# Optimization experiments

Measured on AMD Instinct MI355X. Metric: run time of the kernel, lower is better.

Reference implementation:

```python
import jax, jax.numpy as jnp
import numpy as np

CONF_THRES = 0.4
IOU_THRES = 0.45
MAX_DET = 1000
MAX_WH = 7680.0  # class offset for non-agnostic NMS (yolov5 convention)
K = 2048         # pre-NMS candidate cap (>= MAX_DET)


def setup_inputs() -> dict:
    key = jax.random.key(0)
    k1, k2, k3, k4 = jax.random.split(key, 4)
    # uint8-valued image, stored as int32 (values 0..255)
    img = jax.random.randint(k1, (640, 640, 3), 0, 256, dtype=jnp.int32)
    B, N, NC = 8, 25200, 80
    xy = jax.random.uniform(k2, (B, N, 2)) * 640.0          # box centers in pixels
    wh = jax.random.uniform(k3, (B, N, 2)) * 80.0 + 4.0     # box sizes
    sc = jax.random.uniform(k4, (B, N, 1 + NC))             # objectness + class scores
    pred = jnp.concatenate([xy, wh, sc], axis=-1)           # [B, N, 85]
    return {"img": img, "pred": pred}


def _xywh2xyxy(x):
    xy, wh = x[..., :2], x[..., 2:4]
    return jnp.concatenate([xy - wh * 0.5, xy + wh * 0.5], axis=-1)


def _box_iou(a, b):
    # a: [K,4], b: [K,4] in xyxy
    lt = jnp.maximum(a[:, None, :2], b[None, :, :2])
    rb = jnp.minimum(a[:, None, 2:], b[None, :, 2:])
    wh = jnp.clip(rb - lt, 0.0)
    inter = wh[..., 0] * wh[..., 1]
    area_a = (a[:, 2] - a[:, 0]) * (a[:, 3] - a[:, 1])
    area_b = (b[:, 2] - b[:, 0]) * (b[:, 3] - b[:, 1])
    return inter / (area_a[:, None] + area_b[None, :] - inter + 1e-7)


def _nms_single(p):
    # p: [N, 5+nc]
    boxes = _xywh2xyxy(p[:, :4])                 # [N,4]
    conf_all = p[:, 5:] * p[:, 4:5]              # obj * cls
    conf = jnp.max(conf_all, axis=-1)            # best-class confidence [N]
    cls = jnp.argmax(conf_all, axis=-1).astype(p.dtype)
    scores = jnp.where(conf > CONF_THRES, conf, -1.0)
    # top-K candidates (score-sorted, padding gets score -1)
    top_s, idx = jax.lax.top_k(scores, K)
    b = boxes[idx]                               # [K,4] raw boxes
    c = cls[idx]                                 # [K] class ids (float)
    b_off = b + (c * MAX_WH)[:, None]            # class-offset boxes (agnostic_nms=False)
    iou = _box_iou(b_off, b_off)                 # [K,K]
    keep = top_s > CONF_THRES
    ar = jnp.arange(K)

    def body(i, keep):
        sup = keep[i] & (iou[i] > IOU_THRES) & (ar > i)
        return keep & jnp.logical_not(sup)

    keep = jax.lax.fori_loop(0, K, body, keep)
    fs = jnp.where(keep, top_s, -1.0)
    sel_s, sel = jax.lax.top_k(fs, MAX_DET)
    det = jnp.concatenate([b[sel], sel_s[:, None], c[sel][:, None]], axis=-1)  # [MAX_DET,6]
    return jnp.where((sel_s > CONF_THRES)[:, None], det, 0.0)


def reference(img, pred):
    # process_image: HWC -> CHW, BGR->RGB flip, float, /255, add batch dim
    x = img.astype(jnp.float32).transpose(2, 0, 1)[::-1] / 255.0
    x = x[None]                                  # [1,3,640,640]
    det = jax.vmap(_nms_single)(pred)[0]         # non_max_suppression(pred, ...)[0]
    return det, x
```

## Files before the change

### kernel.cpp

```cpp
#include <hip/hip_runtime.h>
#include <stdint.h>

#define N_ANCH 25200
#define NCLS   80
#define KSEL   2048
#define MAXDET 1000
#define CONF_T 0.4f
#define IOU_T  0.45f
#define MAX_WH 7680.0f
#define HBINS  512
#define HBASE  0xBE00u
#define NCAND_MAX 4096
#define NSB    788
#define NIB    400
#define SUPCAP 224

#define WS_SELSCORE  0
#define WS_SELBOX    8192
#define WS_DETCAND   40960
#define WS_CNT       92160
#define WS_KEYS      92480
#define WS_CLS       193280
#define WS_MASK      294912
#define WS_MTT       819200
#define WS_F         1343488
#define WS_DONE      1343744
#define WS_CAND      294912

#define ST_U32(p, v) __hip_atomic_store((p), (v), __ATOMIC_RELAXED, __HIP_MEMORY_SCOPE_AGENT)

__global__ void __launch_bounds__(256)
prep_kernel(const float* __restrict__ pred0, uint32_t* __restrict__ keys,
            int* __restrict__ cls, uint32_t* __restrict__ cnt,
            uint32_t* __restrict__ fglob, uint32_t* __restrict__ done) {
    int tid = threadIdx.x;
    if (blockIdx.x == 0) {
        if (tid < 64) fglob[tid] = 0u;
        if (tid == 64) *cnt = 0u;
        if (tid == 65) *done = 0u;
    }
    int lane = tid & 63, wave = tid >> 6;
    int g = lane >> 3, l = lane & 7;
    int a = blockIdx.x * 32 + wave * 8 + g;
    if (a >= N_ANCH) return;
    const float* p = pred0 + (size_t)a * 85;
    float obj = p[4];
    float v = -1e30f; int ci = 0;
    #pragma unroll
    for (int k = 0; k < 10; ++k) {
        int c = l + 8 * k;
        float x = p[5 + c] * obj;
        if (x > v) { v = x; ci = c; }
    }
    #pragma unroll
    for (int m = 1; m < 8; m <<= 1) {
        float ov = __shfl_xor(v, m, 64);
        int   oc = __shfl_xor(ci, m, 64);
        if (ov > v || (ov == v && oc < ci)) { v = ov; ci = oc; }
    }
    if (l == 0) {
        float score = (v > CONF_T) ? v : -1.0f;
        uint32_t bits = __float_as_uint(score);
        uint32_t key = (bits & 0x80000000u) ? ~bits : (bits | 0x80000000u);
        keys[a] = key; cls[a] = ci;
    }
}

__global__ void __launch_bounds__(256)
compact_kernel(const uint32_t* __restrict__ keys, uint32_t* __restrict__ cnt,
               unsigned long long* __restrict__ cand,
               const int* __restrict__ img, float* __restrict__ xout) {
    __shared__ uint32_t h[HBINS];
    __shared__ uint32_t s_lim;
    __shared__ int wtot[4];
    __shared__ int s_base;
    int tid = threadIdx.x;

    if (blockIdx.x >= 25) {
        int i = (blockIdx.x - 25) * 256 + tid;
        const int4* im4 = (const int4*)(img + (size_t)i * 12);
        int4 va = im4[0], vb4 = im4[1], vc = im4[2];
        int p0 = i * 4;
        float4 o0 = make_float4((float)va.z / 255.0f, (float)vb4.y / 255.0f,
                                (float)vc.x / 255.0f, (float)vc.w / 255.0f);
        float4 o1 = make_float4((float)va.y / 255.0f, (float)vb4.x / 255.0f,
                                (float)vb4.w / 255.0f, (float)vc.z / 255.0f);
        float4 o2 = make_float4((float)va.x / 255.0f, (float)va.w / 255.0f,
                                (float)vb4.z / 255.0f, (float)vc.y / 255.0f);
        *(float4*)(xout + p0)          = o0;
        *(float4*)(xout + 409600 + p0) = o1;
        *(float4*)(xout + 819200 + p0) = o2;
        return;
    }

    int lane = tid & 63, wv = tid >> 6;
    for (int b = tid; b < HBINS; b += 256) h[b] = 0u;
    if (tid == 0) s_lim = (HBASE << 16);
    __syncthreads();
    for (int i = tid; i < N_ANCH / 4; i += 256) {
        uint4 kk = ((const uint4*)keys)[i];
        if (kk.x >= (HBASE << 16)) atomicAdd(&h[(kk.x >> 16) - HBASE], 1u);
        if (kk.y >= (HBASE << 16)) atomicAdd(&h[(kk.y >> 16) - HBASE], 1u);
        if (kk.z >= (HBASE << 16)) atomicAdd(&h[(kk.z >> 16) - HBASE], 1u);
        if (kk.w >= (HBASE << 16)) atomicAdd(&h[(kk.w >> 16) - HBASE], 1u);
    }
    __syncthreads();
    for (int off = 1; off < HBINS; off <<= 1) {
        uint32_t a0 = h[tid] + ((tid + off < HBINS) ? h[tid + off] : 0u);
        uint32_t a1 = h[tid + 256] + ((tid + 256 + off < HBINS) ? h[tid + 256 + off] : 0u);
        __syncthreads();
        h[tid] = a0; h[tid + 256] = a1;
        __syncthreads();
    }
    for (int b = tid; b < HBINS; b += 256) {
        uint32_t sb  = h[b];
        uint32_t sb1 = (b < HBINS - 1) ? h[b + 1] : 0u;
        if (sb >= KSEL && sb1 < KSEL) s_lim = (uint32_t)(HBASE + b) << 16;
    }
    __syncthreads();
    uint32_t lim = s_lim;

    int i = blockIdx.x * 256 + tid;
    bool valid = (i < N_ANCH / 4);
    uint32_t ks[4] = {0, 0, 0, 0};
    int cm = 0;
    if (valid) {
        uint4 kk = ((const uint4*)keys)[i];
        ks[0] = kk.x; ks[1] = kk.y; ks[2] = kk.z; ks[3] = kk.w;
        #pragma unroll
        for (int j = 0; j < 4; ++j) cm += (ks[j] >= lim) ? 1 : 0;
    }
    int pre = cm;
    #pragma unroll
    for (int o = 1; o < 64; o <<= 1) {
        int v = __shfl_up(pre, o, 64);
        if (lane >= o) pre += v;
    }
    if (lane == 63) wtot[wv] = pre;
    __syncthreads();
    if (tid == 0) {
        int t = 0;
        #pragma unroll
        for (int w = 0; w < 4; ++w) { int x = wtot[w]; wtot[w] = t; t += x; }
        s_base = (t > 0) ? (int)atomicAdd(cnt, (uint32_t)t) : 0;
    }
    __syncthreads();
    int pos = s_base + wtot[wv] + (pre - cm);
    if (valid) {
        #pragma unroll
        for (int j = 0; j < 4; ++j) {
            if (ks[j] >= lim) {
                if (pos < NCAND_MAX)
                    cand[pos] = ((unsigned long long)ks[j] << 32)
                              | (uint32_t)(~(uint32_t)(i * 4 + j));
                ++pos;
            }
        }
    }
}

__global__ void __launch_bounds__(256)
rank_kernel(const uint32_t* __restrict__ cnt, const unsigned long long* __restrict__ cand,
            const float* __restrict__ pred0, const int* __restrict__ cls,
            float* __restrict__ sel_score, float4* __restrict__ selbox,
            float* __restrict__ det_cand) {
    __shared__ unsigned long long s_it[NCAND_MAX];
    __shared__ int s_n;
    int tid = threadIdx.x;
    if (tid == 0) s_n = (int)min(*cnt, (uint32_t)NCAND_MAX);
    __syncthreads();
    int n = s_n;
    int base = blockIdx.x * 32;
    if (base >= n) return;
    for (int i = tid; i < n; i += 256) s_it[i] = cand[i];
    __syncthreads();
    int grp = tid >> 4, s16 = tid & 15;
    #pragma unroll
    for (int o = 0; o < 2; ++o) {
        int it = base + grp + o * 16;
        if (it >= n) break;
        unsigned long long mine = s_it[it];
        int c = 0;
        for (int t = s16; t < n; t += 16)
            c += (s_it[t] > mine) ? 1 : 0;
        #pragma unroll
        for (int m = 1; m < 16; m <<= 1) c += __shfl_xor(c, m, 64);
        if (s16 == 0 && c < KSEL) {
            uint32_t key = (uint32_t)(mine >> 32);
            int ai = (int)(~(uint32_t)mine);
            uint32_t fb = (key & 0x80000000u) ? (key & 0x7FFFFFFFu) : ~key;
            float score = __uint_as_float(fb);
            const float* p = pred0 + (size_t)ai * 85;
            float x = p[0], y = p[1], w = p[2], hh = p[3];
            float x1 = x - w * 0.5f, y1 = y - hh * 0.5f;
            float x2 = x + w * 0.5f, y2 = y + hh * 0.5f;
            float cf = (float)cls[ai];
            float off = cf * MAX_WH;
            selbox[c] = make_float4(x1 + off, y1 + off, x2 + off, y2 + off);
            float* dc = det_cand + (size_t)c * 6;
            dc[0] = x1; dc[1] = y1; dc[2] = x2; dc[3] = y2; dc[4] = score; dc[5] = cf;
            sel_score[c] = score;
        }
    }
}

__global__ void __launch_bounds__(256)
mask_nms_kernel(const float4* __restrict__ selbox, uint32_t* __restrict__ MT,
                uint32_t* __restrict__ MTT, uint32_t* __restrict__ fglob,
                uint32_t* __restrict__ done, const float* __restrict__ sel_score,
                const float* __restrict__ det_cand, float* __restrict__ det) {
    __shared__ __align__(16) uint32_t sup[SUPCAP * 64];
    __shared__ float4 jb[32];
    __shared__ uint32_t f_s[64];
    __shared__ int rowlist[SUPCAP];
    __shared__ int s_R;
    __shared__ int s_last;
    int tid = threadIdx.x;
    int lane = tid & 63, wv = tid >> 6;
    int wi = blockIdx.x >> 3, rg = blockIdx.x & 7;

    if (tid < 32) jb[tid] = selbox[wi * 32 + tid];
    __syncthreads();
    int row = rg * 256 + tid;
    float4 a = selbox[row];
    float areaA = (a.z - a.x) * (a.w - a.y);
    uint32_t bits = 0;
    #pragma unroll 4
    for (int b = 0; b < 32; ++b) {
        int j = wi * 32 + b;
        if (j > row) {
            float4 q = jb[b];
            float lx = fmaxf(a.x, q.x), ly = fmaxf(a.y, q.y);
            float rx = fminf(a.z, q.z), ry = fminf(a.w, q.w);
            float ww = fmaxf(rx - lx, 0.0f), hh = fmaxf(ry - ly, 0.0f);
            float inter = ww * hh;
            float areaB = (q.z - q.x) * (q.w - q.y);
            float iou = inter / (areaA + areaB - inter + 1e-7f);
            if (iou > IOU_T) bits |= (1u << b);
        }
    }
    ST_U32(&MT[(size_t)wi * 2048 + row], bits);
    ST_U32(&MTT[(size_t)row * 64 + wi], bits);
    unsigned long long bm = __ballot(bits != 0u);
    if (lane == 0) {
        int wbase = rg * 8 + wv * 2;
        uint32_t lo = (uint32_t)bm, hi = (uint32_t)(bm >> 32);
        if (lo) atomicOr(&fglob[wbase], lo);
        if (hi) atomicOr(&fglob[wbase + 1], hi);
    }

    __syncthreads();
    if (tid == 0) {
        uint32_t p = __hip_atomic_fetch_add(done, 1u, __ATOMIC_ACQ_REL,
                                            __HIP_MEMORY_SCOPE_AGENT);
        s_last = (p == 511u);
    }
    __syncthreads();
    if (!s_last) return;
    __threadfence();

    if (tid < 64) {
        uint32_t fw = fglob[tid];
        f_s[tid] = fw;
        int cnt1 = __popc(fw);
        int pre = cnt1;
        for (int o = 1; o < 64; o <<= 1) {
            int v = __shfl_up(pre, o, 64);
            if (tid >= o) pre += v;
        }
        int r = pre - cnt1;
        while (fw) {
            int b = __ffs(fw) - 1; fw &= fw - 1;
            if (r < SUPCAP) rowlist[r] = tid * 32 + b;
            ++r;
        }
        if (tid == 63) s_R = pre;
    }
    __syncthreads();
    int R = s_R;
    bool sparse = (R <= SUPCAP);
    if (sparse) {
        int s = tid >> 6, ln = tid & 63;
        while (s + 12 < R) {
            uint32_t a0 = MTT[(size_t)rowlist[s]      * 64 + ln];
            uint32_t a1 = MTT[(size_t)rowlist[s + 4]  * 64 + ln];
            uint32_t a2 = MTT[(size_t)rowlist[s + 8]  * 64 + ln];
            uint32_t a3 = MTT[(size_t)rowlist[s + 12] * 64 + ln];
            sup[s * 64 + ln] = a0;        sup[(s + 4) * 64 + ln] = a1;
            sup[(s + 8) * 64 + ln] = a2;  sup[(s + 12) * 64 + ln] = a3;
            s += 16;
        }
        for (; s < R; s += 4)
            sup[s * 64 + ln] = MTT[(size_t)rowlist[s] * 64 + ln];
    }
    __syncthreads();
    if (tid >= 64) return;

    uint32_t removed = 0;
    #pragma unroll
    for (int b = 0; b < 32; ++b)
        if (!(sel_score[lane * 32 + b] > CONF_T)) removed |= (1u << b);

    if (sparse) {
        int slot = 0;
        for (int w = 0; w < 64; ++w) {
            uint32_t fb = f_s[w];
            while (fb) {
                int b = __ffs(fb) - 1; fb &= fb - 1;
                uint32_t rv = __shfl((int)removed, w, 64);
                if (!((rv >> b) & 1u))
                    removed |= sup[slot * 64 + lane];
                ++slot;
            }
        }
    } else {
        for (int c = 0; c < 64; ++c) {
            uint32_t rw[32];
            #pragma unroll 8
            for (int b = 0; b < 32; ++b)
                rw[b] = MT[(size_t)lane * 2048 + c * 32 + b];
            uint32_t keptmask = 0;
            if (lane == c) {
                uint32_t myrem = removed;
                #pragma unroll
                for (int b = 0; b < 32; ++b)
                    if (!((myrem >> b) & 1u)) { keptmask |= (1u << b); myrem |= rw[b]; }
            }
            keptmask = __shfl(keptmask, c, 64);
            #pragma unroll
            for (int b = 0; b < 32; ++b)
                if ((keptmask >> b) & 1u) removed |= rw[b];
        }
    }

    uint32_t kw = ~removed;
    int cnt2 = __popc(kw);
    int pre = cnt2;
    for (int o = 1; o < 64; o <<= 1) {
        int v = __shfl_up(pre, o, 64);
        if (lane >= o) pre += v;
    }
    int excl = pre - cnt2;
    int total = __shfl(pre, 63, 64);

    int r = excl;
    for (int b = 0; b < 32; ++b) {
        if ((kw >> b) & 1u) {
            if (r < MAXDET) {
                const float* src = det_cand + (size_t)(lane * 32 + b) * 6;
                float* dst = det + (size_t)r * 6;
                for (int j = 0; j < 6; ++j) dst[j] = src[j];
            }
            ++r;
        }
    }
    int start = total < MAXDET ? total : MAXDET;
    for (int z = start + lane; z < MAXDET; z += 64) {
        float* dst = det + (size_t)z * 6;
        for (int j = 0; j < 6; ++j) dst[j] = 0.0f;
    }
}

extern "C" void kernel_launch(void* const* d_in, const int* in_sizes, int n_in,
                              void* d_out, int out_size, void* d_ws, size_t ws_size,
                              hipStream_t stream) {
    const int*   img  = (const int*)d_in[0];
    const float* pred = (const float*)d_in[1];
    float* out = (float*)d_out;
    char* ws = (char*)d_ws;

    float*    sel_score = (float*)(ws + WS_SELSCORE);
    float4*   selbox    = (float4*)(ws + WS_SELBOX);
    float*    det_cand  = (float*)(ws + WS_DETCAND);
    uint32_t* cnt       = (uint32_t*)(ws + WS_CNT);
    uint32_t* keys      = (uint32_t*)(ws + WS_KEYS);
    int*      cls       = (int*)(ws + WS_CLS);
    uint32_t* MT        = (uint32_t*)(ws + WS_MASK);
    uint32_t* MTT       = (uint32_t*)(ws + WS_MTT);
    uint32_t* fglob     = (uint32_t*)(ws + WS_F);
    uint32_t* done      = (uint32_t*)(ws + WS_DONE);
    unsigned long long* cand = (unsigned long long*)(ws + WS_CAND);
    float* xout = out + MAXDET * 6;

    prep_kernel<<<NSB, 256, 0, stream>>>(pred, keys, cls, cnt, fglob, done);
    compact_kernel<<<25 + NIB, 256, 0, stream>>>(keys, cnt, cand, img, xout);
    rank_kernel<<<128, 256, 0, stream>>>(cnt, cand, pred, cls,
                                         sel_score, selbox, det_cand);
    mask_nms_kernel<<<512, 256, 0, stream>>>(selbox, MT, MTT, fglob, done,
                                             sel_score, det_cand, out);
}
```

Baseline: 154.9 us.

## Restructure pipeline: fuse compaction into rank, split mask and NMS kernels

```diff
diff --git a/kernel.cpp b/kernel.cpp
--- a/kernel.cpp
+++ b/kernel.cpp
@@ -18,66 +18,22 @@
 #define WS_SELSCORE  0
 #define WS_SELBOX    8192
 #define WS_DETCAND   40960
-#define WS_CNT       92160
 #define WS_KEYS      92480
 #define WS_CLS       193280
 #define WS_MASK      294912
 #define WS_MTT       819200
 #define WS_F         1343488
-#define WS_DONE      1343744
-#define WS_CAND      294912
-
-#define ST_U32(p, v) __hip_atomic_store((p), (v), __ATOMIC_RELAXED, __HIP_MEMORY_SCOPE_AGENT)
 
 __global__ void __launch_bounds__(256)
-prep_kernel(const float* __restrict__ pred0, uint32_t* __restrict__ keys,
-            int* __restrict__ cls, uint32_t* __restrict__ cnt,
-            uint32_t* __restrict__ fglob, uint32_t* __restrict__ done) {
+prep_img_kernel(const float* __restrict__ pred0, const int* __restrict__ img,
+                float* __restrict__ xout, uint32_t* __restrict__ keys,
+                int* __restrict__ cls, uint32_t* __restrict__ fglob) {
     int tid = threadIdx.x;
-    if (blockIdx.x == 0) {
-        if (tid < 64) fglob[tid] = 0u;
-        if (tid == 64) *cnt = 0u;
-        if (tid == 65) *done = 0u;
-    }
-    int lane = tid & 63, wave = tid >> 6;
-    int g = lane >> 3, l = lane & 7;
-    int a = blockIdx.x * 32 + wave * 8 + g;
-    if (a >= N_ANCH) return;
-    const float* p = pred0 + (size_t)a * 85;
-    float obj = p[4];
-    float v = -1e30f; int ci = 0;
-    #pragma unroll
-    for (int k = 0; k < 10; ++k) {
-        int c = l + 8 * k;
-        float x = p[5 + c] * obj;
-        if (x > v) { v = x; ci = c; }
-    }
-    #pragma unroll
-    for (int m = 1; m < 8; m <<= 1) {
-        float ov = __shfl_xor(v, m, 64);
-        int   oc = __shfl_xor(ci, m, 64);
-        if (ov > v || (ov == v && oc < ci)) { v = ov; ci = oc; }
-    }
-    if (l == 0) {
-        float score = (v > CONF_T) ? v : -1.0f;
-        uint32_t bits = __float_as_uint(score);
-        uint32_t key = (bits & 0x80000000u) ? ~bits : (bits | 0x80000000u);
-        keys[a] = key; cls[a] = ci;
-    }
-}
-
-__global__ void __launch_bounds__(256)
-compact_kernel(const uint32_t* __restrict__ keys, uint32_t* __restrict__ cnt,
-               unsigned long long* __restrict__ cand,
-               const int* __restrict__ img, float* __restrict__ xout) {
-    __shared__ uint32_t h[HBINS];
-    __shared__ uint32_t s_lim;
-    __shared__ int wtot[4];
-    __shared__ int s_base;
-    int tid = threadIdx.x;
-
-    if (blockIdx.x >= 25) {
-        int i = (blockIdx.x - 25) * 256 + tid;
+    int bid = blockIdx.x;
+    if (bid == 0 && tid < 64) fglob[tid] = 0u;
+
+    if (bid >= NSB) {
+        int i = (bid - NSB) * 256 + tid;
         const int4* im4 = (const int4*)(img + (size_t)i * 12);
         int4 va = im4[0], vb4 = im4[1], vc = im4[2];
         int p0 = i * 4;
@@ -93,7 +49,43 @@
         return;
     }
 
-    int lane = tid & 63, wv = tid >> 6;
+    int lane = tid & 63, wave = tid >> 6;
+    int g = lane >> 3, l = lane & 7;
+    int a = bid * 32 + wave * 8 + g;
+    if (a >= N_ANCH) return;
+    const float* p = pred0 + (size_t)a * 85;
+    float obj = p[4];
+    float v = -1e30f; int ci = 0;
+    #pragma unroll
+    for (int k = 0; k < 10; ++k) {
+        int c = l + 8 * k;
+        float x = p[5 + c] * obj;
+        if (x > v) { v = x; ci = c; }
+    }
+    #pragma unroll
+    for (int m = 1; m < 8; m <<= 1) {
+        float ov = __shfl_xor(v, m, 64);
+        int   oc = __shfl_xor(ci, m, 64);
+        if (ov > v || (ov == v && oc < ci)) { v = ov; ci = oc; }
+    }
+    if (l == 0) {
+        float score = (v > CONF_T) ? v : -1.0f;
+        uint32_t bits = __float_as_uint(score);
+        uint32_t key = (bits & 0x80000000u) ? ~bits : (bits | 0x80000000u);
+        keys[a] = key; cls[a] = ci;
+    }
+}
+
+__global__ void __launch_bounds__(256)
+rank_kernel(const uint32_t* __restrict__ keys, const float* __restrict__ pred0,
+            const int* __restrict__ cls, float* __restrict__ sel_score,
+            float4* __restrict__ selbox, float* __restrict__ det_cand) {
+    __shared__ uint32_t h[HBINS];
+    __shared__ unsigned long long s_it[NCAND_MAX];
+    __shared__ uint32_t wt[101];
+    __shared__ uint32_t s_lim;
+    int tid = threadIdx.x, lane = tid & 63, wv = tid >> 6;
+
     for (int b = tid; b < HBINS; b += 256) h[b] = 0u;
     if (tid == 0) s_lim = (HBASE << 16);
     __syncthreads();
@@ -120,60 +112,65 @@
     __syncthreads();
     uint32_t lim = s_lim;
 
-    int i = blockIdx.x * 256 + tid;
-    bool valid = (i < N_ANCH / 4);
-    uint32_t ks[4] = {0, 0, 0, 0};
-    int cm = 0;
-    if (valid) {
-        uint4 kk = ((const uint4*)keys)[i];
-        ks[0] = kk.x; ks[1] = kk.y; ks[2] = kk.z; ks[3] = kk.w;
+    #pragma unroll 5
+    for (int it = 0; it < 25; ++it) {
+        int i = it * 256 + tid;
+        int cm = 0;
+        if (i < N_ANCH / 4) {
+            uint4 kk = ((const uint4*)keys)[i];
+            cm = (kk.x >= lim) + (kk.y >= lim) + (kk.z >= lim) + (kk.w >= lim);
+        }
+        int pre = cm;
         #pragma unroll
-        for (int j = 0; j < 4; ++j) cm += (ks[j] >= lim) ? 1 : 0;
-    }
-    int pre = cm;
-    #pragma unroll
-    for (int o = 1; o < 64; o <<= 1) {
-        int v = __shfl_up(pre, o, 64);
-        if (lane >= o) pre += v;
-    }
-    if (lane == 63) wtot[wv] = pre;
+        for (int o = 1; o < 64; o <<= 1) {
+            int v = __shfl_up(pre, o, 64);
+            if (lane >= o) pre += v;
+        }
+        if (lane == 63) wt[it * 4 + wv] = (uint32_t)pre;
+    }
     __syncthreads();
     if (tid == 0) {
-        int t = 0;
+        uint32_t t = 0;
+        for (int k = 0; k < 100; ++k) { uint32_t x = wt[k]; wt[k] = t; t += x; }
+        wt[100] = t;
+    }
+    __syncthreads();
+    int n = (int)min(wt[100], (uint32_t)NCAND_MAX);
+
+    #pragma unroll 5
+    for (int it = 0; it < 25; ++it) {
+        int i = it * 256 + tid;
+        uint32_t ks[4] = {0, 0, 0, 0};
+        int cm = 0;
+        if (i < N_ANCH / 4) {
+            uint4 kk = ((const uint4*)keys)[i];
+            ks[0] = kk.x; ks[1] = kk.y; ks[2] = kk.z; ks[3] = kk.w;
+            #pragma unroll
+            for (int j = 0; j < 4; ++j) cm += (ks[j] >= lim) ? 1 : 0;
+        }
+        int pre = cm;
         #pragma unroll
-        for (int w = 0; w < 4; ++w) { int x = wtot[w]; wtot[w] = t; t += x; }
-        s_base = (t > 0) ? (int)atomicAdd(cnt, (uint32_t)t) : 0;
-    }
-    __syncthreads();
-    int pos = s_base + wtot[wv] + (pre - cm);
-    if (valid) {
-        #pragma unroll
-        for (int j = 0; j < 4; ++j) {
-            if (ks[j] >= lim) {
-                if (pos < NCAND_MAX)
-                    cand[pos] = ((unsigned long long)ks[j] << 32)
-                              | (uint32_t)(~(uint32_t)(i * 4 + j));
-                ++pos;
+        for (int o = 1; o < 64; o <<= 1) {
+            int v = __shfl_up(pre, o, 64);
+            if (lane >= o) pre += v;
+        }
+        int pos = (int)wt[it * 4 + wv] + (pre - cm);
+        if (i < N_ANCH / 4) {
+            #pragma unroll
+            for (int j = 0; j < 4; ++j) {
+                if (ks[j] >= lim) {
+                    if (pos < NCAND_MAX)
+                        s_it[pos] = ((unsigned long long)ks[j] << 32)
+                                  | (uint32_t)(~(uint32_t)(i * 4 + j));
+                    ++pos;
+                }
             }
         }
     }
-}
-
-__global__ void __launch_bounds__(256)
-rank_kernel(const uint32_t* __restrict__ cnt, const unsigned long long* __restrict__ cand,
-            const float* __restrict__ pred0, const int* __restrict__ cls,
-            float* __restrict__ sel_score, float4* __restrict__ selbox,
-            float* __restrict__ det_cand) {
-    __shared__ unsigned long long s_it[NCAND_MAX];
-    __shared__ int s_n;
-    int tid = threadIdx.x;
-    if (tid == 0) s_n = (int)min(*cnt, (uint32_t)NCAND_MAX);
-    __syncthreads();
-    int n = s_n;
+    __syncthreads();
+
     int base = blockIdx.x * 32;
     if (base >= n) return;
-    for (int i = tid; i < n; i += 256) s_it[i] = cand[i];
-    __syncthreads();
     int grp = tid >> 4, s16 = tid & 15;
     #pragma unroll
     for (int o = 0; o < 2; ++o) {
@@ -205,16 +202,9 @@
 }
 
 __global__ void __launch_bounds__(256)
-mask_nms_kernel(const float4* __restrict__ selbox, uint32_t* __restrict__ MT,
-                uint32_t* __restrict__ MTT, uint32_t* __restrict__ fglob,
-                uint32_t* __restrict__ done, const float* __restrict__ sel_score,
-                const float* __restrict__ det_cand, float* __restrict__ det) {
-    __shared__ __align__(16) uint32_t sup[SUPCAP * 64];
+mask_kernel(const float4* __restrict__ selbox, uint32_t* __restrict__ MT,
+            uint32_t* __restrict__ MTT, uint32_t* __restrict__ fglob) {
     __shared__ float4 jb[32];
-    __shared__ uint32_t f_s[64];
-    __shared__ int rowlist[SUPCAP];
-    __shared__ int s_R;
-    __shared__ int s_last;
     int tid = threadIdx.x;
     int lane = tid & 63, wv = tid >> 6;
     int wi = blockIdx.x >> 3, rg = blockIdx.x & 7;
@@ -239,8 +229,8 @@
             if (iou > IOU_T) bits |= (1u << b);
         }
     }
-    ST_U32(&MT[(size_t)wi * 2048 + row], bits);
-    ST_U32(&MTT[(size_t)row * 64 + wi], bits);
+    MT[(size_t)wi * 2048 + row] = bits;
+    MTT[(size_t)row * 64 + wi] = bits;
     unsigned long long bm = __ballot(bits != 0u);
     if (lane == 0) {
         int wbase = rg * 8 + wv * 2;
@@ -248,16 +238,17 @@
         if (lo) atomicOr(&fglob[wbase], lo);
         if (hi) atomicOr(&fglob[wbase + 1], hi);
     }
-
-    __syncthreads();
-    if (tid == 0) {
-        uint32_t p = __hip_atomic_fetch_add(done, 1u, __ATOMIC_ACQ_REL,
-                                            __HIP_MEMORY_SCOPE_AGENT);
-        s_last = (p == 511u);
-    }
-    __syncthreads();
-    if (!s_last) return;
-    __threadfence();
+}
+
+__global__ void __launch_bounds__(256)
+nms_kernel(const uint32_t* __restrict__ MT, const uint32_t* __restrict__ MTT,
+           const uint32_t* __restrict__ fglob, const float* __restrict__ sel_score,
+           const float* __restrict__ det_cand, float* __restrict__ det) {
+    __shared__ __align__(16) uint32_t sup[SUPCAP * 64];
+    __shared__ uint32_t f_s[64];
+    __shared__ int rowlist[SUPCAP];
+    __shared__ int s_R;
+    int tid = threadIdx.x;
 
     if (tid < 64) {
         uint32_t fw = fglob[tid];
@@ -296,6 +287,7 @@
     __syncthreads();
     if (tid >= 64) return;
 
+    int lane = tid;
     uint32_t removed = 0;
     #pragma unroll
     for (int b = 0; b < 32; ++b)
@@ -372,20 +364,16 @@
     float*    sel_score = (float*)(ws + WS_SELSCORE);
     float4*   selbox    = (float4*)(ws + WS_SELBOX);
     float*    det_cand  = (float*)(ws + WS_DETCAND);
-    uint32_t* cnt       = (uint32_t*)(ws + WS_CNT);
     uint32_t* keys      = (uint32_t*)(ws + WS_KEYS);
     int*      cls       = (int*)(ws + WS_CLS);
     uint32_t* MT        = (uint32_t*)(ws + WS_MASK);
     uint32_t* MTT       = (uint32_t*)(ws + WS_MTT);
     uint32_t* fglob     = (uint32_t*)(ws + WS_F);
-    uint32_t* done      = (uint32_t*)(ws + WS_DONE);
-    unsigned long long* cand = (unsigned long long*)(ws + WS_CAND);
     float* xout = out + MAXDET * 6;
 
-    prep_kernel<<<NSB, 256, 0, stream>>>(pred, keys, cls, cnt, fglob, done);
-    compact_kernel<<<25 + NIB, 256, 0, stream>>>(keys, cnt, cand, img, xout);
-    rank_kernel<<<128, 256, 0, stream>>>(cnt, cand, pred, cls,
+    prep_img_kernel<<<NSB + NIB, 256, 0, stream>>>(pred, img, xout, keys, cls, fglob);
+    rank_kernel<<<128, 256, 0, stream>>>(keys, pred, cls,
                                          sel_score, selbox, det_cand);
-    mask_nms_kernel<<<512, 256, 0, stream>>>(selbox, MT, MTT, fglob, done,
-                                             sel_score, det_cand, out);
-}
+    mask_kernel<<<512, 256, 0, stream>>>(selbox, MT, MTT, fglob);
+    nms_kernel<<<1, 256, 0, stream>>>(MT, MTT, fglob, sel_score, det_cand, out);
+}
```

Result: slower. 164.7 us (+6.3%).

## Widen rank kernel parallelism and split mask/NMS into separate kernels

Applied to the files above, without the earlier changes.

```diff
diff --git a/kernel.cpp b/kernel.cpp
--- a/kernel.cpp
+++ b/kernel.cpp
@@ -14,6 +14,7 @@
 #define NSB    788
 #define NIB    400
 #define SUPCAP 224
+#define RKB    512
 
 #define WS_SELSCORE  0
 #define WS_SELBOX    8192
@@ -24,20 +25,16 @@
 #define WS_MASK      294912
 #define WS_MTT       819200
 #define WS_F         1343488
-#define WS_DONE      1343744
 #define WS_CAND      294912
-
-#define ST_U32(p, v) __hip_atomic_store((p), (v), __ATOMIC_RELAXED, __HIP_MEMORY_SCOPE_AGENT)
 
 __global__ void __launch_bounds__(256)
 prep_kernel(const float* __restrict__ pred0, uint32_t* __restrict__ keys,
             int* __restrict__ cls, uint32_t* __restrict__ cnt,
-            uint32_t* __restrict__ fglob, uint32_t* __restrict__ done) {
+            uint32_t* __restrict__ fglob) {
     int tid = threadIdx.x;
     if (blockIdx.x == 0) {
         if (tid < 64) fglob[tid] = 0u;
         if (tid == 64) *cnt = 0u;
-        if (tid == 65) *done = 0u;
     }
     int lane = tid & 63, wave = tid >> 6;
     int g = lane >> 3, l = lane & 7;
@@ -170,22 +167,22 @@
     if (tid == 0) s_n = (int)min(*cnt, (uint32_t)NCAND_MAX);
     __syncthreads();
     int n = s_n;
-    int base = blockIdx.x * 32;
+    int base = blockIdx.x * 8;
     if (base >= n) return;
+    #pragma unroll 4
     for (int i = tid; i < n; i += 256) s_it[i] = cand[i];
     __syncthreads();
-    int grp = tid >> 4, s16 = tid & 15;
-    #pragma unroll
-    for (int o = 0; o < 2; ++o) {
-        int it = base + grp + o * 16;
-        if (it >= n) break;
+    int grp = tid >> 5, s32 = tid & 31;
+    int it = base + grp;
+    if (it < n) {
         unsigned long long mine = s_it[it];
         int c = 0;
-        for (int t = s16; t < n; t += 16)
+        #pragma unroll 8
+        for (int t = s32; t < n; t += 32)
             c += (s_it[t] > mine) ? 1 : 0;
         #pragma unroll
-        for (int m = 1; m < 16; m <<= 1) c += __shfl_xor(c, m, 64);
-        if (s16 == 0 && c < KSEL) {
+        for (int m = 1; m < 32; m <<= 1) c += __shfl_xor(c, m, 64);
+        if (s32 == 0 && c < KSEL) {
             uint32_t key = (uint32_t)(mine >> 32);
             int ai = (int)(~(uint32_t)mine);
             uint32_t fb = (key & 0x80000000u) ? (key & 0x7FFFFFFFu) : ~key;
@@ -205,16 +202,9 @@
 }
 
 __global__ void __launch_bounds__(256)
-mask_nms_kernel(const float4* __restrict__ selbox, uint32_t* __restrict__ MT,
-                uint32_t* __restrict__ MTT, uint32_t* __restrict__ fglob,
-                uint32_t* __restrict__ done, const float* __restrict__ sel_score,
-                const float* __restrict__ det_cand, float* __restrict__ det) {
-    __shared__ __align__(16) uint32_t sup[SUPCAP * 64];
+mask_kernel(const float4* __restrict__ selbox, uint32_t* __restrict__ MT,
+            uint32_t* __restrict__ MTT, uint32_t* __restrict__ fglob) {
     __shared__ float4 jb[32];
-    __shared__ uint32_t f_s[64];
-    __shared__ int rowlist[SUPCAP];
-    __shared__ int s_R;
-    __shared__ int s_last;
     int tid = threadIdx.x;
     int lane = tid & 63, wv = tid >> 6;
     int wi = blockIdx.x >> 3, rg = blockIdx.x & 7;
@@ -239,8 +229,8 @@
             if (iou > IOU_T) bits |= (1u << b);
         }
     }
-    ST_U32(&MT[(size_t)wi * 2048 + row], bits);
-    ST_U32(&MTT[(size_t)row * 64 + wi], bits);
+    MT[(size_t)wi * 2048 + row] = bits;
+    MTT[(size_t)row * 64 + wi] = bits;
     unsigned long long bm = __ballot(bits != 0u);
     if (lane == 0) {
         int wbase = rg * 8 + wv * 2;
@@ -248,16 +238,17 @@
         if (lo) atomicOr(&fglob[wbase], lo);
         if (hi) atomicOr(&fglob[wbase + 1], hi);
     }
-
-    __syncthreads();
-    if (tid == 0) {
-        uint32_t p = __hip_atomic_fetch_add(done, 1u, __ATOMIC_ACQ_REL,
-                                            __HIP_MEMORY_SCOPE_AGENT);
-        s_last = (p == 511u);
-    }
-    __syncthreads();
-    if (!s_last) return;
-    __threadfence();
+}
+
+__global__ void __launch_bounds__(256)
+nms_kernel(const uint32_t* __restrict__ MT, const uint32_t* __restrict__ MTT,
+           const uint32_t* __restrict__ fglob, const float* __restrict__ sel_score,
+           const float* __restrict__ det_cand, float* __restrict__ det) {
+    __shared__ __align__(16) uint32_t sup[SUPCAP * 64];
+    __shared__ uint32_t f_s[64];
+    __shared__ int rowlist[SUPCAP];
+    __shared__ int s_R;
+    int tid = threadIdx.x;
 
     if (tid < 64) {
         uint32_t fw = fglob[tid];
@@ -296,6 +287,7 @@
     __syncthreads();
     if (tid >= 64) return;
 
+    int lane = tid;
     uint32_t removed = 0;
     #pragma unroll
     for (int b = 0; b < 32; ++b)
@@ -378,14 +370,13 @@
     uint32_t* MT        = (uint32_t*)(ws + WS_MASK);
     uint32_t* MTT       = (uint32_t*)(ws + WS_MTT);
     uint32_t* fglob     = (uint32_t*)(ws + WS_F);
-    uint32_t* done      = (uint32_t*)(ws + WS_DONE);
     unsigned long long* cand = (unsigned long long*)(ws + WS_CAND);
     float* xout = out + MAXDET * 6;
 
-    prep_kernel<<<NSB, 256, 0, stream>>>(pred, keys, cls, cnt, fglob, done);
+    prep_kernel<<<NSB, 256, 0, stream>>>(pred, keys, cls, cnt, fglob);
     compact_kernel<<<25 + NIB, 256, 0, stream>>>(keys, cnt, cand, img, xout);
-    rank_kernel<<<128, 256, 0, stream>>>(cnt, cand, pred, cls,
+    rank_kernel<<<RKB, 256, 0, stream>>>(cnt, cand, pred, cls,
                                          sel_score, selbox, det_cand);
-    mask_nms_kernel<<<512, 256, 0, stream>>>(selbox, MT, MTT, fglob, done,
-                                             sel_score, det_cand, out);
-}
+    mask_kernel<<<512, 256, 0, stream>>>(selbox, MT, MTT, fglob);
+    nms_kernel<<<1, 256, 0, stream>>>(MT, MTT, fglob, sel_score, det_cand, out);
+}
```

After: 134.7 us, median of 2. 1.15x faster.
